# Optimization experiments

Measured on AMD Instinct MI355X. Metric: run time of the kernel, lower is better.

## Reference

```python
import jax, jax.numpy as jnp
import numpy as np

N_NODES = 50000


def setup_inputs() -> dict:
    key = jax.random.key(0)
    k1, k2, k3, k4, k5, k6 = jax.random.split(key, 6)
    N, E, D, F = 50000, 800000, 512, 256
    feature_ori = jax.random.normal(k1, (N, D), dtype=jnp.float32)
    feature_aug = jax.random.normal(k2, (N, D), dtype=jnp.float32)
    edge_row = jax.random.randint(k3, (E,), 0, N, dtype=jnp.int32)
    edge_col = jax.random.randint(k4, (E,), 0, N, dtype=jnp.int32)
    edge_val = jax.random.uniform(k5, (E,), dtype=jnp.float32)
    # kaiming-uniform-ish init for weight, zeros for bias (as in reset_parameters)
    bound = float(np.sqrt(6.0 / D))
    weight = jax.random.uniform(k6, (D, F), dtype=jnp.float32, minval=-bound, maxval=bound)
    bias = jnp.zeros((F,), dtype=jnp.float32)
    return {
        "feature_ori": feature_ori,
        "feature_aug": feature_aug,
        "edge_row": edge_row,
        "edge_col": edge_col,
        "edge_val": edge_val,
        "weight": weight,
        "bias": bias,
    }


def _branch(feat, weight, bias, edge_row, edge_col, edge_val):
    # support = X @ W  -> [N, F]
    support = feat @ weight
    # sparse aggregation: out[i] = sum_{e: row[e]=i} val[e] * support[col[e]]
    msgs = edge_val[:, None] * support[edge_col]          # [E, F]
    out = jax.ops.segment_sum(msgs, edge_row, num_segments=N_NODES)
    return jax.nn.relu(out + bias)


def reference(feature_ori, feature_aug, edge_row, edge_col, edge_val, weight, bias):
    out_ori = _branch(feature_ori, weight, bias, edge_row, edge_col, edge_val)
    out_aug = _branch(feature_aug, weight, bias, edge_row, edge_col, edge_val)
    return (out_ori, out_aug)
```

## Files before the change

### kernel.cpp

```cpp
#include <hip/hip_runtime.h>
#include <hip/hip_bf16.h>

#define NNODES 50000
#define NEDGES 800000
#define DIN    512
#define FOUT   256

typedef __attribute__((ext_vector_type(8))) short short8;
typedef __attribute__((ext_vector_type(4))) float f32x4;
typedef __attribute__((ext_vector_type(4))) unsigned int u32x4;
typedef __attribute__((ext_vector_type(4))) unsigned short usv4;
typedef __attribute__((ext_vector_type(8))) unsigned short usv8;

static __device__ __forceinline__ unsigned short f2bf(float f) {
    unsigned int u = __float_as_uint(f);
    u += 0x7FFF + ((u >> 16) & 1);
    return (unsigned short)(u >> 16);
}
static __device__ __forceinline__ float bf2f(unsigned short h) {
    return __uint_as_float(((unsigned int)h) << 16);
}

__global__ void prep_kernel(const float* __restrict__ W, unsigned short* __restrict__ Wt,
                            const int* __restrict__ row, int* __restrict__ cnt) {
    int b = blockIdx.x;
    if (b < 512) {
        int o = b * 256 + threadIdx.x;
        int n = o >> 9, k = o & 511;
        Wt[o] = f2bf(W[k * FOUT + n]);
    } else {
        int e = (b - 512) * 256 + threadIdx.x;
        if (e < NEDGES) atomicAdd(&cnt[row[e]], 1);
    }
}

__global__ void scan_partial(const int* __restrict__ cnt, int* __restrict__ partial) {
    __shared__ int sm[256];
    int i = blockIdx.x * 256 + threadIdx.x;
    int v = (i < NNODES) ? cnt[i] : 0;
    sm[threadIdx.x] = v; __syncthreads();
    for (int s = 128; s > 0; s >>= 1) {
        if (threadIdx.x < s) sm[threadIdx.x] += sm[threadIdx.x + s];
        __syncthreads();
    }
    if (threadIdx.x == 0) partial[blockIdx.x] = sm[0];
}

__global__ void scan_exclusive_small(int* __restrict__ partial, int nb) {
    __shared__ int sm[256];
    int t = threadIdx.x;
    int v = (t < nb) ? partial[t] : 0;
    sm[t] = v; __syncthreads();
    for (int off = 1; off < 256; off <<= 1) {
        int add = (t >= off) ? sm[t - off] : 0;
        __syncthreads();
        sm[t] += add;
        __syncthreads();
    }
    if (t < nb) partial[t] = sm[t] - v;
}

__global__ void scan_write(const int* __restrict__ cnt, const int* __restrict__ partial,
                           int* __restrict__ row_start, int* __restrict__ cursor) {
    __shared__ int sm[256];
    int t = threadIdx.x;
    int i = blockIdx.x * 256 + t;
    int v = (i < NNODES) ? cnt[i] : 0;
    sm[t] = v; __syncthreads();
    for (int off = 1; off < 256; off <<= 1) {
        int add = (t >= off) ? sm[t - off] : 0;
        __syncthreads();
        sm[t] += add;
        __syncthreads();
    }
    if (i < NNODES) {
        int rs = partial[blockIdx.x] + sm[t] - v;
        row_start[i] = rs;
        cursor[i] = rs;
    }
    if (i == 0) row_start[NNODES] = NEDGES;
}

__global__ void scatter_kernel(const int* __restrict__ row, const int* __restrict__ col,
                               const float* __restrict__ val,
                               int* __restrict__ cursor, unsigned int* __restrict__ cv) {
    int e = blockIdx.x * 256 + threadIdx.x;
    if (e < NEDGES) {
        int r = row[e];
        int pos = atomicAdd(&cursor[r], 1);
        unsigned int vb = f2bf(val[e]);
        cv[pos] = (vb << 16) | (unsigned int)col[e];
    }
}

__global__ __launch_bounds__(512, 2)
void gemm_kernel(const float* __restrict__ Xo, const float* __restrict__ Xa,
                 const unsigned short* __restrict__ Wt,
                 unsigned short* __restrict__ S) {
    __shared__ __align__(16) unsigned short As[2][128][40];
    __shared__ __align__(16) unsigned short Bs[2][256][40];
    const int tid = threadIdx.x;
    const int branch = blockIdx.z;
    const float* __restrict__ X = branch ? Xa : Xo;
    const int boff = branch * 256;
    const int m_base = blockIdx.x * 128;
    const int lane = tid & 63, wave = tid >> 6;
    const int wm = (wave >> 2) * 64, wn = (wave & 3) * 64;
    const int quad = lane >> 4, r16 = lane & 15;

    f32x4 acc[4][4] = {};

    const int colf  = (tid & 7) * 4;
    const int rbase = tid >> 3;
    const int kseg  = (tid & 3) * 8;
    const int nrow  = tid >> 2;

    const int gm0 = m_base + rbase;
    const int gm1 = m_base + 64 + rbase;
    const bool va0 = gm0 < NNODES, va1 = gm1 < NNODES;
    const float* pA0 = &X[(long)gm0 * DIN + colf];
    const float* pA1 = &X[(long)gm1 * DIN + colf];
    const unsigned short* pB0 = &Wt[(long)nrow * DIN + kseg];
    const unsigned short* pB1 = &Wt[(long)(128 + nrow) * DIN + kseg];

    f32x4 fa0, fa1; u32x4 ub0, ub1;

#define GEMM_LOAD(K0)                                                          \
    do {                                                                       \
        fa0 = va0 ? __builtin_nontemporal_load((const f32x4*)(pA0 + (K0)))     \
                  : (f32x4)0.f;                                                \
        fa1 = va1 ? __builtin_nontemporal_load((const f32x4*)(pA1 + (K0)))     \
                  : (f32x4)0.f;                                                \
        ub0 = *(const u32x4*)(pB0 + (K0));                                     \
        ub1 = *(const u32x4*)(pB1 + (K0));                                     \
    } while (0)

#define GEMM_WRITE(B)                                                          \
    do {                                                                       \
        usv4 h0; h0.x = f2bf(fa0[0]); h0.y = f2bf(fa0[1]);                     \
        h0.z = f2bf(fa0[2]); h0.w = f2bf(fa0[3]);                              \
        *(usv4*)&As[B][rbase][colf] = h0;                                      \
        usv4 h1; h1.x = f2bf(fa1[0]); h1.y = f2bf(fa1[1]);                     \
        h1.z = f2bf(fa1[2]); h1.w = f2bf(fa1[3]);                              \
        *(usv4*)&As[B][64 + rbase][colf] = h1;                                 \
        *(u32x4*)&Bs[B][nrow][kseg] = ub0;                                     \
        *(u32x4*)&Bs[B][128 + nrow][kseg] = ub1;                               \
    } while (0)

#define GEMM_COMPUTE(B)                                                        \
    do {                                                                       \
        short8 a_frag[4], b_frag[4];                                           \
        _Pragma("unroll")                                                      \
        for (int mi = 0; mi < 4; mi++)                                         \
            a_frag[mi] = *(const short8*)&As[B][wm + mi * 16 + r16][quad * 8]; \
        _Pragma("unroll")                                                      \
        for (int ni = 0; ni < 4; ni++)                                         \
            b_frag[ni] = *(const short8*)&Bs[B][wn + ni * 16 + r16][quad * 8]; \
        _Pragma("unroll")                                                      \
        for (int mi = 0; mi < 4; mi++)                                         \
            _Pragma("unroll")                                                  \
            for (int ni = 0; ni < 4; ni++)                                     \
                acc[mi][ni] = __builtin_amdgcn_mfma_f32_16x16x32_bf16(         \
                    a_frag[mi], b_frag[ni], acc[mi][ni], 0, 0, 0);             \
    } while (0)

    GEMM_LOAD(0);
    GEMM_WRITE(0);
    __syncthreads();

    for (int k0 = 0; k0 < DIN; k0 += 64) {
        GEMM_LOAD(k0 + 32);
        GEMM_COMPUTE(0);
        GEMM_WRITE(1);
        __syncthreads();
        if (k0 + 64 < DIN) GEMM_LOAD(k0 + 64);
        GEMM_COMPUTE(1);
        if (k0 + 64 < DIN) GEMM_WRITE(0);
        __syncthreads();
    }

#undef GEMM_LOAD
#undef GEMM_WRITE
#undef GEMM_COMPUTE

    #pragma unroll
    for (int mi = 0; mi < 4; mi++) {
        #pragma unroll
        for (int rr = 0; rr < 4; rr++) {
            int m = m_base + wm + mi * 16 + quad * 4 + rr;
            if (m < NNODES) {
                #pragma unroll
                for (int ni = 0; ni < 4; ni++) {
                    int n = wn + ni * 16 + r16;
                    S[(long)m * 512 + boff + n] = f2bf(acc[mi][ni][rr]);
                }
            }
        }
    }
}

__global__ __launch_bounds__(256)
void aggregate_pass(const int* __restrict__ row_start,
                    const unsigned int* __restrict__ cv,
                    const unsigned short* __restrict__ S,
                    const float* __restrict__ bias, float* __restrict__ out,
                    const int half) {
    const int node = __builtin_amdgcn_readfirstlane(blockIdx.x * 4 + (threadIdx.x >> 6));
    if (node >= NNODES) return;
    const int lane = threadIdx.x & 63;
    const int fl = (lane & 31) * 8;
    const unsigned int sub = lane >> 5;
    const long soff = (long)half * 256 + fl;
    const int s = row_start[node], e = row_start[node + 1];

    float a0 = 0.f, a1 = 0.f, a2 = 0.f, a3 = 0.f;
    float a4 = 0.f, a5 = 0.f, a6 = 0.f, a7 = 0.f;

#define PLOAD(CW0, CW1, Q)                                                     \
    do {                                                                       \
        unsigned int cw_ = sub ? (CW1) : (CW0);                                \
        Q = *(const usv8*)&S[(long)(cw_ & 0xFFFFu) * 512 + soff];              \
    } while (0)

#define PFMA(CW0, CW1, Q)                                                      \
    do {                                                                       \
        unsigned int cw_ = sub ? (CW1) : (CW0);                                \
        float v = bf2f((unsigned short)(cw_ >> 16));                           \
        a0 = fmaf(v, bf2f((Q)[0]), a0); a1 = fmaf(v, bf2f((Q)[1]), a1);        \
        a2 = fmaf(v, bf2f((Q)[2]), a2); a3 = fmaf(v, bf2f((Q)[3]), a3);        \
        a4 = fmaf(v, bf2f((Q)[4]), a4); a5 = fmaf(v, bf2f((Q)[5]), a5);        \
        a6 = fmaf(v, bf2f((Q)[6]), a6); a7 = fmaf(v, bf2f((Q)[7]), a7);        \
    } while (0)

#define LOADG(C0, C1, C2, C3, C4, C5, C6, C7, Q0, Q1, Q2, Q3, I)               \
    do {                                                                       \
        C0 = cv[(I)];     C1 = cv[(I) + 1]; C2 = cv[(I) + 2]; C3 = cv[(I) + 3];\
        C4 = cv[(I) + 4]; C5 = cv[(I) + 5]; C6 = cv[(I) + 6]; C7 = cv[(I) + 7];\
        PLOAD(C0, C1, Q0); PLOAD(C2, C3, Q1);                                  \
        PLOAD(C4, C5, Q2); PLOAD(C6, C7, Q3);                                  \
    } while (0)

#define FMAG(C0, C1, C2, C3, C4, C5, C6, C7, Q0, Q1, Q2, Q3)                   \
    do {                                                                       \
        PFMA(C0, C1, Q0); PFMA(C2, C3, Q1);                                    \
        PFMA(C4, C5, Q2); PFMA(C6, C7, Q3);                                    \
    } while (0)

    unsigned int c0, c1, c2, c3, c4, c5, c6, c7;
    unsigned int d0, d1, d2, d3, d4, d5, d6, d7;
    usv8 qa0, qa1, qa2, qa3, qb0, qb1, qb2, qb3;

    int idx = s;
    int r = (e - s) >> 3;
    if (r > 0) {
        LOADG(c0, c1, c2, c3, c4, c5, c6, c7, qa0, qa1, qa2, qa3, idx); idx += 8; r--;
        while (r >= 2) {
            LOADG(d0, d1, d2, d3, d4, d5, d6, d7, qb0, qb1, qb2, qb3, idx); idx += 8;
            FMAG(c0, c1, c2, c3, c4, c5, c6, c7, qa0, qa1, qa2, qa3);
            LOADG(c0, c1, c2, c3, c4, c5, c6, c7, qa0, qa1, qa2, qa3, idx); idx += 8;
            FMAG(d0, d1, d2, d3, d4, d5, d6, d7, qb0, qb1, qb2, qb3);
            r -= 2;
        }
        if (r == 1) {
            LOADG(d0, d1, d2, d3, d4, d5, d6, d7, qb0, qb1, qb2, qb3, idx); idx += 8;
            FMAG(c0, c1, c2, c3, c4, c5, c6, c7, qa0, qa1, qa2, qa3);
            FMAG(d0, d1, d2, d3, d4, d5, d6, d7, qb0, qb1, qb2, qb3);
        } else {
            FMAG(c0, c1, c2, c3, c4, c5, c6, c7, qa0, qa1, qa2, qa3);
        }
    }
    for (; idx + 2 <= e; idx += 2) {
        unsigned int w0 = cv[idx], w1 = cv[idx + 1];
        usv8 q;
        PLOAD(w0, w1, q);
        PFMA(w0, w1, q);
    }
    if (idx < e) {
        unsigned int w = cv[idx];
        usv8 q = *(const usv8*)&S[(long)(w & 0xFFFFu) * 512 + soff];
        float v = sub ? 0.f : bf2f((unsigned short)(w >> 16));
        a0 = fmaf(v, bf2f(q[0]), a0); a1 = fmaf(v, bf2f(q[1]), a1);
        a2 = fmaf(v, bf2f(q[2]), a2); a3 = fmaf(v, bf2f(q[3]), a3);
        a4 = fmaf(v, bf2f(q[4]), a4); a5 = fmaf(v, bf2f(q[5]), a5);
        a6 = fmaf(v, bf2f(q[6]), a6); a7 = fmaf(v, bf2f(q[7]), a7);
    }

#undef PLOAD
#undef PFMA
#undef LOADG
#undef FMAG

    a0 += __shfl_xor(a0, 32); a1 += __shfl_xor(a1, 32);
    a2 += __shfl_xor(a2, 32); a3 += __shfl_xor(a3, 32);
    a4 += __shfl_xor(a4, 32); a5 += __shfl_xor(a5, 32);
    a6 += __shfl_xor(a6, 32); a7 += __shfl_xor(a7, 32);

    if (lane < 32) {
        f32x4 b0 = *(const f32x4*)&bias[fl];
        f32x4 b1 = *(const f32x4*)&bias[fl + 4];
        long o = (long)half * NNODES * FOUT + (long)node * FOUT + fl;
        f32x4 r0, r1;
        r0[0] = fmaxf(a0 + b0[0], 0.f); r0[1] = fmaxf(a1 + b0[1], 0.f);
        r0[2] = fmaxf(a2 + b0[2], 0.f); r0[3] = fmaxf(a3 + b0[3], 0.f);
        r1[0] = fmaxf(a4 + b1[0], 0.f); r1[1] = fmaxf(a5 + b1[1], 0.f);
        r1[2] = fmaxf(a6 + b1[2], 0.f); r1[3] = fmaxf(a7 + b1[3], 0.f);
        __builtin_nontemporal_store(r0, (f32x4*)&out[o]);
        __builtin_nontemporal_store(r1, (f32x4*)&out[o + 4]);
    }
}

extern "C" void kernel_launch(void* const* d_in, const int* in_sizes, int n_in,
                              void* d_out, int out_size, void* d_ws, size_t ws_size,
                              hipStream_t stream) {
    const float* Xo   = (const float*)d_in[0];
    const float* Xa   = (const float*)d_in[1];
    const int*   erow = (const int*)d_in[2];
    const int*   ecol = (const int*)d_in[3];
    const float* eval_= (const float*)d_in[4];
    const float* W    = (const float*)d_in[5];
    const float* bias = (const float*)d_in[6];
    float* out = (float*)d_out;

    char* ws = (char*)d_ws;
    unsigned short* S         = (unsigned short*)(ws);
    unsigned short* Wt        = (unsigned short*)(ws + 51200000);
    int*            cnt       = (int*)(ws + 51462144);
    int*            row_start = (int*)(ws + 51662144);
    int*            partial   = (int*)(ws + 51862208);
    unsigned int*   cv        = (unsigned int*)(ws + 51863232);

    (void)in_sizes; (void)n_in; (void)out_size; (void)ws_size;

    hipMemsetAsync(cnt, 0, 200000, stream);
    prep_kernel<<<3637, 256, 0, stream>>>(W, Wt, erow, cnt);
    scan_partial<<<196, 256, 0, stream>>>(cnt, partial);
    scan_exclusive_small<<<1, 256, 0, stream>>>(partial, 196);
    scan_write<<<196, 256, 0, stream>>>(cnt, partial, row_start, cnt);
    scatter_kernel<<<3125, 256, 0, stream>>>(erow, ecol, eval_, cnt, cv);

    dim3 gg(391, 1, 2);
    gemm_kernel<<<gg, 512, 0, stream>>>(Xo, Xa, Wt, S);

    aggregate_pass<<<12500, 256, 0, stream>>>(row_start, cv, S, bias, out, 0);
    aggregate_pass<<<12500, 256, 0, stream>>>(row_start, cv, S, bias, out, 1);
}
```

Measured before the change: 482.5 us.

## Deepen GEMM global-load prefetch to two stages with lighter barriers

```diff
diff --git a/kernel.cpp b/kernel.cpp
--- a/kernel.cpp
+++ b/kernel.cpp
@@ -110,41 +110,40 @@
 
     f32x4 acc[4][4] = {};
 
-    const int colf  = (tid & 7) * 4;
-    const int rbase = tid >> 3;
-    const int kseg  = (tid & 3) * 8;
-    const int nrow  = tid >> 2;
-
-    const int gm0 = m_base + rbase;
-    const int gm1 = m_base + 64 + rbase;
-    const bool va0 = gm0 < NNODES, va1 = gm1 < NNODES;
-    const float* pA0 = &X[(long)gm0 * DIN + colf];
-    const float* pA1 = &X[(long)gm1 * DIN + colf];
+    const int arow = tid >> 2;
+    const int acol = (tid & 3) * 8;
+    const int kseg = (tid & 3) * 8;
+    const int nrow = tid >> 2;
+
+    const int gm = m_base + arow;
+    const bool va = gm < NNODES;
+    const float* pA = &X[(long)gm * DIN + acol];
     const unsigned short* pB0 = &Wt[(long)nrow * DIN + kseg];
     const unsigned short* pB1 = &Wt[(long)(128 + nrow) * DIN + kseg];
 
-    f32x4 fa0, fa1; u32x4 ub0, ub1;
-
-#define GEMM_LOAD(K0)                                                          \
-    do {                                                                       \
-        fa0 = va0 ? __builtin_nontemporal_load((const f32x4*)(pA0 + (K0)))     \
-                  : (f32x4)0.f;                                                \
-        fa1 = va1 ? __builtin_nontemporal_load((const f32x4*)(pA1 + (K0)))     \
-                  : (f32x4)0.f;                                                \
-        ub0 = *(const u32x4*)(pB0 + (K0));                                     \
-        ub1 = *(const u32x4*)(pB1 + (K0));                                     \
-    } while (0)
-
-#define GEMM_WRITE(B)                                                          \
-    do {                                                                       \
-        usv4 h0; h0.x = f2bf(fa0[0]); h0.y = f2bf(fa0[1]);                     \
-        h0.z = f2bf(fa0[2]); h0.w = f2bf(fa0[3]);                              \
-        *(usv4*)&As[B][rbase][colf] = h0;                                      \
-        usv4 h1; h1.x = f2bf(fa1[0]); h1.y = f2bf(fa1[1]);                     \
-        h1.z = f2bf(fa1[2]); h1.w = f2bf(fa1[3]);                              \
-        *(usv4*)&As[B][64 + rbase][colf] = h1;                                 \
-        *(u32x4*)&Bs[B][nrow][kseg] = ub0;                                     \
-        *(u32x4*)&Bs[B][128 + nrow][kseg] = ub1;                               \
+    f32x4 fa0A, fa1A, fa0B, fa1B;
+    u32x4 ub0A, ub1A, ub0B, ub1B;
+
+#define GEMM_LOAD(SET, K0)                                                     \
+    do {                                                                       \
+        fa0##SET = va ? __builtin_nontemporal_load((const f32x4*)(pA + (K0)))  \
+                      : (f32x4)0.f;                                            \
+        fa1##SET = va ? __builtin_nontemporal_load((const f32x4*)(pA + (K0) + 4))\
+                      : (f32x4)0.f;                                            \
+        ub0##SET = *(const u32x4*)(pB0 + (K0));                                \
+        ub1##SET = *(const u32x4*)(pB1 + (K0));                                \
+    } while (0)
+
+#define GEMM_WRITE(SET, B)                                                     \
+    do {                                                                       \
+        usv8 h;                                                                \
+        h[0] = f2bf(fa0##SET[0]); h[1] = f2bf(fa0##SET[1]);                    \
+        h[2] = f2bf(fa0##SET[2]); h[3] = f2bf(fa0##SET[3]);                    \
+        h[4] = f2bf(fa1##SET[0]); h[5] = f2bf(fa1##SET[1]);                    \
+        h[6] = f2bf(fa1##SET[2]); h[7] = f2bf(fa1##SET[3]);                    \
+        *(usv8*)&As[B][arow][acol] = h;                                        \
+        *(u32x4*)&Bs[B][nrow][kseg] = ub0##SET;                                \
+        *(u32x4*)&Bs[B][128 + nrow][kseg] = ub1##SET;                          \
     } while (0)
 
 #define GEMM_COMPUTE(B)                                                        \
@@ -164,24 +163,36 @@
                     a_frag[mi], b_frag[ni], acc[mi][ni], 0, 0, 0);             \
     } while (0)
 
-    GEMM_LOAD(0);
-    GEMM_WRITE(0);
-    __syncthreads();
-
-    for (int k0 = 0; k0 < DIN; k0 += 64) {
-        GEMM_LOAD(k0 + 32);
+#define GEMM_BARRIER()                                                         \
+    do {                                                                       \
+        asm volatile("s_waitcnt lgkmcnt(0)" ::: "memory");                     \
+        __builtin_amdgcn_s_barrier();                                          \
+        __builtin_amdgcn_sched_barrier(0);                                     \
+    } while (0)
+
+    GEMM_LOAD(A, 0);
+    GEMM_WRITE(A, 0);
+    GEMM_LOAD(A, 32);
+    GEMM_BARRIER();
+
+    #pragma unroll
+    for (int t = 0; t < 16; t += 2) {
+        if (t + 2 < 16) GEMM_LOAD(B, (t + 2) * 32);
         GEMM_COMPUTE(0);
-        GEMM_WRITE(1);
-        __syncthreads();
-        if (k0 + 64 < DIN) GEMM_LOAD(k0 + 64);
+        GEMM_WRITE(A, 1);
+        GEMM_BARRIER();
+        if (t + 3 < 16) GEMM_LOAD(A, (t + 3) * 32);
         GEMM_COMPUTE(1);
-        if (k0 + 64 < DIN) GEMM_WRITE(0);
-        __syncthreads();
+        if (t + 2 < 16) {
+            GEMM_WRITE(B, 0);
+            GEMM_BARRIER();
+        }
     }
 
 #undef GEMM_LOAD
 #undef GEMM_WRITE
 #undef GEMM_COMPUTE
+#undef GEMM_BARRIER
 
     #pragma unroll
     for (int mi = 0; mi < 4; mi++) {
```

Measured after the change: 469.1 us. -2.8%, faster.
